# Kernel tuning notes

Hardware: AMD Instinct MI355X
Metric: run time of the kernel (lower is better)

The kernel has to match this reference:

```python
import jax, jax.numpy as jnp
import numpy as np

HIDDEN_DIM = 2048
LAYER_IDX = 12
NUM_LAYERS = 24
BATCH, SEQ_LEN = 4, 4096

def _init_time_decay(layer_idx, num_layers, hidden_dim):
    ratio = layer_idx / max(num_layers - 1, 1)
    i = np.arange(hidden_dim, dtype=np.float32)
    channel_ratio = i / max(hidden_dim - 1, 1)
    zigzag = ((i + 1) % 3 - 1) * 0.1
    decay = -5 + 4.5 * (ratio * 0.3 + channel_ratio * 0.7) + zigzag
    return jnp.asarray(decay, dtype=jnp.float32)

def setup_inputs() -> dict:
    key = jax.random.key(0)
    k1, k2 = jax.random.split(key)
    k = jax.random.normal(k1, (BATCH, SEQ_LEN, HIDDEN_DIM), dtype=jnp.float32)
    v = jax.random.normal(k2, (BATCH, SEQ_LEN, HIDDEN_DIM), dtype=jnp.float32)
    time_decay = _init_time_decay(LAYER_IDX, NUM_LAYERS, HIDDEN_DIM)
    time_first = jnp.zeros((HIDDEN_DIM,), dtype=jnp.float32)
    return {"k": k, "v": v, "time_decay": time_decay, "time_first": time_first}

def reference(k, v, time_decay, time_first):
    # w = -exp(time_decay); per-step decay factor ew = exp(w)
    ew = jnp.exp(-jnp.exp(time_decay))          # (H,)
    u = time_first                              # (H,)
    eps = 1e-8

    # scan over time: carry (a, b) each (B, H)
    def step(carry, kv_t):
        a, b = carry
        k_t, v_t = kv_t                         # (B, H) each
        ek = jnp.exp(k_t)
        euk = jnp.exp(u + k_t)
        wkv_t = (a + euk * v_t) / (b + euk + eps)
        new_a = ew * a + ek * v_t
        new_b = ew * b + ek
        return (new_a, new_b), wkv_t

    B, T, H = k.shape
    a0 = jnp.zeros((B, H), dtype=k.dtype)
    b0 = jnp.zeros((B, H), dtype=k.dtype)
    # time-major for scan
    kT = jnp.transpose(k, (1, 0, 2))            # (T, B, H)
    vT = jnp.transpose(v, (1, 0, 2))
    (a, b), outT = jax.lax.scan(step, (a0, b0), (kT, vT))
    output = jnp.transpose(outT, (1, 0, 2))     # (B, T, H)
    return output, a, b
```

## Files before the change

### kernel.cpp

```cpp
#include <hip/hip_runtime.h>
#include <math.h>
#include <stdint.h>

#define B 4
#define T 4096
#define H 2048
#define TT 256
#define NT (T / TT)
#define NBAND (H / 32)
#define THREADS 512
#define NSUB 16
#define SUBL (TT / NSUB)

typedef const __attribute__((address_space(1))) uint32_t* gas_ptr;
typedef __attribute__((address_space(3))) uint32_t* las_ptr;

__device__ __forceinline__ void stage8(const float* gbase, float* lbase, int lane) {
    __builtin_amdgcn_global_load_lds(
        (gas_ptr)(const void*)(gbase + (lane >> 3) * H + (lane & 7) * 4),
        (las_ptr)(void*)lbase, 16, 0, 0);
}

__global__ __launch_bounds__(THREADS)
void wkv_fused_kernel(const float* __restrict__ kg,
                      const float* __restrict__ vg,
                      const float* __restrict__ td,
                      const float* __restrict__ tf,
                      float* __restrict__ out) {
    __shared__ float lk[2][TT][32];
    __shared__ float lv[2][TT][32];
    __shared__ float sa[NSUB][32];
    __shared__ float sb[NSUB][32];

    int band = blockIdx.x & (NBAND - 1);
    int b    = blockIdx.x >> 6;
    int tid  = threadIdx.x;
    int lane = tid & 63;
    int wv   = tid >> 6;
    int ch   = tid & 31;
    int sub  = tid >> 5;

    const float* kbase = kg + (size_t)b * T * H + band * 32;
    const float* vbase = vg + (size_t)b * T * H + band * 32;
    float* obase       = out + (size_t)b * T * H + band * 32;

    int h = band * 32 + ch;
    float ew = expf(-expf(td[h]));
    float eu = expf(tf[h]);

    float e2 = ew * ew, e4 = e2 * e2, e8 = e4 * e4;
    float ewL  = e8 * e8;
    float el2  = ewL * ewL;
    float el4  = el2 * el2;
    float el8  = el4 * el4;
    float ewT  = el8 * el8;
    float ewpow = 1.0f;
    if (sub & 1) ewpow *= ewL;
    if (sub & 2) ewpow *= el2;
    if (sub & 4) ewpow *= el4;
    if (sub & 8) ewpow *= el8;

    float Ra = 0.f, Rb = 0.f;

#define ISSUE(tile, bufi)                                                   \
    {                                                                       \
        _Pragma("unroll")                                                   \
        for (int ii = 0; ii < 4; ++ii) {                                    \
            int i = wv * 4 + ii;                                            \
            stage8(kbase + ((size_t)(tile) * TT + 8 * i) * H,               \
                   &lk[bufi][8 * i][0], lane);                              \
            stage8(vbase + ((size_t)(tile) * TT + 8 * i) * H,               \
                   &lv[bufi][8 * i][0], lane);                              \
        }                                                                   \
    }

    ISSUE(0, 0);
    for (int j = 0; j < NT; ++j) {
        const int cur = j & 1;
        if (j + 1 < NT) {
            ISSUE(j + 1, cur ^ 1);
            asm volatile("s_waitcnt vmcnt(8)" ::: "memory");
        } else {
            asm volatile("s_waitcnt vmcnt(0)" ::: "memory");
        }
        __builtin_amdgcn_s_barrier();

        float la = 0.f, lb = 0.f;
#pragma unroll
        for (int i = 0; i < SUBL; ++i) {
            int t = sub * SUBL + i;
            float kk = lk[cur][t][ch];
            float vv = lv[cur][t][ch];
            float ek  = expf(kk);
            float ekv = ek * vv;
            lk[cur][t][ch] = ek;
            lv[cur][t][ch] = ekv;
            la = ew * la + ekv;
            lb = ew * lb + ek;
        }
        sa[sub][ch] = la;
        sb[sub][ch] = lb;
        asm volatile("s_waitcnt lgkmcnt(0)" ::: "memory");
        __builtin_amdgcn_s_barrier();

        float pa = 0.f, pb = 0.f, ta = 0.f, tb = 0.f;
#pragma unroll
        for (int s = 0; s < NSUB; ++s) {
            float xa = sa[s][ch];
            float xb = sb[s][ch];
            ta = ewL * ta + xa;
            tb = ewL * tb + xb;
            bool use = (s < sub);
            pa = use ? (ewL * pa + xa) : pa;
            pb = use ? (ewL * pb + xb) : pb;
        }
        float a2 = ewpow * Ra + pa;
        float b2 = ewpow * Rb + pb;
        Ra = ewT * Ra + ta;
        Rb = ewT * Rb + tb;

#pragma unroll
        for (int i = 0; i < SUBL; ++i) {
            int t = sub * SUBL + i;
            float ek  = lk[cur][t][ch];
            float ekv = lv[cur][t][ch];
            float num = a2 + eu * ekv;
            float den = b2 + eu * ek + 1e-8f;
            float inv;
            asm("v_rcp_f32 %0, %1" : "=v"(inv) : "v"(den));
            float r = num * inv;
            __builtin_nontemporal_store(r, obase + ((size_t)j * TT + t) * H + ch);
            a2 = ew * a2 + ekv;
            b2 = ew * b2 + ek;
        }
        __builtin_amdgcn_s_barrier();
    }

    if (tid < 32) {
        size_t so = (size_t)B * T * H;
        out[so + (size_t)b * H + h] = Ra;
        out[so + (size_t)B * H + (size_t)b * H + h] = Rb;
    }
}

extern "C" void kernel_launch(void* const* d_in, const int* in_sizes, int n_in,
                              void* d_out, int out_size, void* d_ws, size_t ws_size,
                              hipStream_t stream) {
    const float* k  = (const float*)d_in[0];
    const float* v  = (const float*)d_in[1];
    const float* td = (const float*)d_in[2];
    const float* tf = (const float*)d_in[3];
    float* out      = (float*)d_out;

    dim3 grid(B * NBAND);
    wkv_fused_kernel<<<grid, dim3(THREADS), 0, stream>>>(k, v, td, tf, out);
}
```

Before: 82.23 us.

## Double block threads and subchunks, pack scan partials, deepen load waits

```diff
diff --git a/kernel.cpp b/kernel.cpp
--- a/kernel.cpp
+++ b/kernel.cpp
@@ -8,8 +8,8 @@
 #define TT 256
 #define NT (T / TT)
 #define NBAND (H / 32)
-#define THREADS 512
-#define NSUB 16
+#define THREADS 1024
+#define NSUB 32
 #define SUBL (TT / NSUB)
 
 typedef const __attribute__((address_space(1))) uint32_t* gas_ptr;
@@ -27,10 +27,9 @@
                       const float* __restrict__ td,
                       const float* __restrict__ tf,
                       float* __restrict__ out) {
-    __shared__ float lk[2][TT][32];
-    __shared__ float lv[2][TT][32];
-    __shared__ float sa[NSUB][32];
-    __shared__ float sb[NSUB][32];
+    __shared__ float  lk[2][TT][32];
+    __shared__ float  lv[2][TT][32];
+    __shared__ float2 sab[NSUB][32];
 
     int band = blockIdx.x & (NBAND - 1);
     int b    = blockIdx.x >> 6;
@@ -48,40 +47,44 @@
     float ew = expf(-expf(td[h]));
     float eu = expf(tf[h]);
 
-    float e2 = ew * ew, e4 = e2 * e2, e8 = e4 * e4;
-    float ewL  = e8 * e8;
-    float el2  = ewL * ewL;
-    float el4  = el2 * el2;
-    float el8  = el4 * el4;
-    float ewT  = el8 * el8;
+    float e2 = ew * ew, e4 = e2 * e2;
+    float ewL  = e4 * e4;
+    float l2   = ewL * ewL;
+    float l4   = l2 * l2;
+    float l8   = l4 * l4;
+    float l16  = l8 * l8;
+    float ewT  = l16 * l16;
     float ewpow = 1.0f;
-    if (sub & 1) ewpow *= ewL;
-    if (sub & 2) ewpow *= el2;
-    if (sub & 4) ewpow *= el4;
-    if (sub & 8) ewpow *= el8;
+    if (sub & 1)  ewpow *= ewL;
+    if (sub & 2)  ewpow *= l2;
+    if (sub & 4)  ewpow *= l4;
+    if (sub & 8)  ewpow *= l8;
+    if (sub & 16) ewpow *= l16;
 
     float Ra = 0.f, Rb = 0.f;
 
 #define ISSUE(tile, bufi)                                                   \
     {                                                                       \
         _Pragma("unroll")                                                   \
-        for (int ii = 0; ii < 4; ++ii) {                                    \
-            int i = wv * 4 + ii;                                            \
-            stage8(kbase + ((size_t)(tile) * TT + 8 * i) * H,               \
-                   &lk[bufi][8 * i][0], lane);                              \
-            stage8(vbase + ((size_t)(tile) * TT + 8 * i) * H,               \
-                   &lv[bufi][8 * i][0], lane);                              \
+        for (int ii = 0; ii < 2; ++ii) {                                    \
+            int g = wv * 2 + ii;                                            \
+            stage8(kbase + ((size_t)(tile) * TT + 8 * g) * H,               \
+                   &lk[bufi][8 * g][0], lane);                              \
+            stage8(vbase + ((size_t)(tile) * TT + 8 * g) * H,               \
+                   &lv[bufi][8 * g][0], lane);                              \
         }                                                                   \
     }
 
     ISSUE(0, 0);
     for (int j = 0; j < NT; ++j) {
         const int cur = j & 1;
-        if (j + 1 < NT) {
-            ISSUE(j + 1, cur ^ 1);
+        if (j + 1 < NT) ISSUE(j + 1, cur ^ 1);
+        if (j == 0) {
+            asm volatile("s_waitcnt vmcnt(4)" ::: "memory");
+        } else if (j + 1 < NT) {
+            asm volatile("s_waitcnt vmcnt(12)" ::: "memory");
+        } else {
             asm volatile("s_waitcnt vmcnt(8)" ::: "memory");
-        } else {
-            asm volatile("s_waitcnt vmcnt(0)" ::: "memory");
         }
         __builtin_amdgcn_s_barrier();
 
@@ -91,28 +94,26 @@
             int t = sub * SUBL + i;
             float kk = lk[cur][t][ch];
             float vv = lv[cur][t][ch];
-            float ek  = expf(kk);
+            float ek  = __expf(kk);
             float ekv = ek * vv;
             lk[cur][t][ch] = ek;
             lv[cur][t][ch] = ekv;
             la = ew * la + ekv;
             lb = ew * lb + ek;
         }
-        sa[sub][ch] = la;
-        sb[sub][ch] = lb;
+        sab[sub][ch] = make_float2(la, lb);
         asm volatile("s_waitcnt lgkmcnt(0)" ::: "memory");
         __builtin_amdgcn_s_barrier();
 
-        float pa = 0.f, pb = 0.f, ta = 0.f, tb = 0.f;
+        float ta = 0.f, tb = 0.f, pa = 0.f, pb = 0.f;
 #pragma unroll
         for (int s = 0; s < NSUB; ++s) {
-            float xa = sa[s][ch];
-            float xb = sb[s][ch];
-            ta = ewL * ta + xa;
-            tb = ewL * tb + xb;
-            bool use = (s < sub);
-            pa = use ? (ewL * pa + xa) : pa;
-            pb = use ? (ewL * pb + xb) : pb;
+            float2 x = sab[s][ch];
+            bool cap = (s == sub);
+            pa = cap ? ta : pa;
+            pb = cap ? tb : pb;
+            ta = ewL * ta + x.x;
+            tb = ewL * tb + x.y;
         }
         float a2 = ewpow * Ra + pa;
         float b2 = ewpow * Rb + pb;
```

Result: faster. 79.72 us (-3.1%).
